# Optimization experiments

Measured on AMD Instinct MI355X. Metric: run time of the kernel, lower is better.

Reference implementation:

```python
import jax, jax.numpy as jnp
import numpy as np

B, S, D, H = 2, 2048, 1024, 16
DK = D // H


def setup_inputs() -> dict:
    key = jax.random.key(0)
    ks = jax.random.split(key, 8)
    Q = jax.random.normal(ks[0], (B, S, D), dtype=jnp.float32)
    K = jax.random.normal(ks[1], (B, S, D), dtype=jnp.float32)
    V = jax.random.normal(ks[2], (B, S, D), dtype=jnp.float32)
    scale = 0.02
    W_q = jax.random.normal(ks[3], (D, D), dtype=jnp.float32) * scale
    W_k = jax.random.normal(ks[4], (D, D), dtype=jnp.float32) * scale
    W_v = jax.random.normal(ks[5], (D, D), dtype=jnp.float32) * scale
    W_o = jax.random.normal(ks[6], (D, D), dtype=jnp.float32) * scale
    b_q = jnp.zeros((D,), jnp.float32)
    b_k = jnp.zeros((D,), jnp.float32)
    b_v = jnp.zeros((D,), jnp.float32)
    b_o = jnp.zeros((D,), jnp.float32)
    # causal mask, broadcastable [1,1,S,S]; mask==0 positions are masked out
    mask = jnp.tril(jnp.ones((S, S), jnp.int32))[None, None, :, :]
    return dict(Q=Q, K=K, V=V, W_q=W_q, b_q=b_q, W_k=W_k, b_k=b_k,
                W_v=W_v, b_v=b_v, W_o=W_o, b_o=b_o, mask=mask)


def reference(Q, K, V, W_q, b_q, W_k, b_k, W_v, b_v, W_o, b_o, mask):
    # linear projections (torch Linear equivalent up to weight layout)
    q = Q @ W_q + b_q   # [B,S,D]
    k = K @ W_k + b_k
    v = V @ W_v + b_v
    # split heads -> [B,H,S,DK]
    q = q.reshape(B, S, H, DK).transpose(0, 2, 1, 3)
    k = k.reshape(B, S, H, DK).transpose(0, 2, 1, 3)
    v = v.reshape(B, S, H, DK).transpose(0, 2, 1, 3)
    # scaled dot-product attention with explicit [B,H,S,S] scores
    scores = jnp.einsum('bhqd,bhkd->bhqk', q, k) / jnp.sqrt(jnp.float32(DK))
    scores = jnp.where(mask == 0, jnp.float32(-1e9), scores)
    attn = jax.nn.softmax(scores, axis=-1)
    out = jnp.einsum('bhqk,bhkd->bhqd', attn, v)
    # merge heads and output projection
    out = out.transpose(0, 2, 1, 3).reshape(B, S, D)
    return out @ W_o + b_o
```

## Files before the change

kernel.cpp:

```cpp
#include <hip/hip_runtime.h>


typedef unsigned short u16;
typedef __attribute__((ext_vector_type(8))) short s8v;
typedef __attribute__((ext_vector_type(4))) float f4v;

#define S_ 2048
#define D_ 1024
#define H_ 16
#define DK_ 64

__device__ __forceinline__ u16 f2bf(float f) {
  unsigned u = __builtin_bit_cast(unsigned, f);
  u += 0x7fffu + ((u >> 16) & 1u);
  return (u16)(u >> 16);
}
__device__ __forceinline__ u16 f2bf_t(float f) {
  return (u16)(__builtin_bit_cast(unsigned, f) >> 16);
}

__device__ __forceinline__ void gld_lds16(const u16* g, u16* l) {
  __builtin_amdgcn_global_load_lds(
      (const __attribute__((address_space(1))) unsigned int*)g,
      (__attribute__((address_space(3))) unsigned int*)l, 16, 0, 0);
}

__global__ __launch_bounds__(256) void prep(
    const float* __restrict__ Q, const float* __restrict__ K, const float* __restrict__ V,
    u16* __restrict__ Qc, u16* __restrict__ Kc, u16* __restrict__ Vc,
    const float* __restrict__ W0, const float* __restrict__ W1,
    const float* __restrict__ W2, const float* __restrict__ W3,
    u16* __restrict__ T0, u16* __restrict__ T1, u16* __restrict__ T2, u16* __restrict__ T3) {
  int bid = blockIdx.x, tid = threadIdx.x;
  if (bid < 3072) {
    int z = bid >> 10, t = bid & 1023;
    const float* s = z == 0 ? Q : z == 1 ? K : V;
    u16*         d = z == 0 ? Qc : z == 1 ? Kc : Vc;
    const int n4 = (2 * S_ * D_) / 4;
    for (int idx = t * 256 + tid; idx < n4; idx += 1024 * 256) {
      float4 f = ((const float4*)s)[idx];
      unsigned lo = (unsigned)f2bf(f.x) | ((unsigned)f2bf(f.y) << 16);
      unsigned hi = (unsigned)f2bf(f.z) | ((unsigned)f2bf(f.w) << 16);
      ((uint2*)d)[idx] = make_uint2(lo, hi);
    }
  } else {
    int wb = bid - 3072;
    int z = wb >> 10, t = wb & 1023;
    const float* W = z == 0 ? W0 : z == 1 ? W1 : z == 2 ? W2 : W3;
    u16*         T = z == 0 ? T0 : z == 1 ? T1 : z == 2 ? T2 : T3;
    __shared__ float tile[32][33];
    int tx = tid & 31, ty = tid >> 5;
    int c0 = (t & 31) * 32, r0 = (t >> 5) * 32;
#pragma unroll
    for (int i = 0; i < 32; i += 8)
      tile[ty + i][tx] = W[(size_t)(r0 + ty + i) * D_ + c0 + tx];
    __syncthreads();
#pragma unroll
    for (int i = 0; i < 32; i += 8)
      T[(size_t)(c0 + ty + i) * D_ + r0 + tx] = f2bf(tile[tx][ty + i]);
  }
}

#define BK_ 64

template <int MI, int NJ, int MODE>
__device__ __forceinline__ void gemm_core(const u16* __restrict__ A, const u16* __restrict__ Bt,
                                          const float* __restrict__ bias, void* __restrict__ out,
                                          float oscale, u16* lds, int m0, int n0) {
  constexpr int BM = MI * 32;
  constexpr int BN = NJ * 32;
  u16* Al = lds;
  u16* Bl = lds + BM * BK_;
  int tid = threadIdx.x;
  int w = tid >> 6, lane = tid & 63, quad = lane >> 4, col = lane & 15;
  int wm = (w >> 1) * (MI * 16), wn = (w & 1) * (NJ * 16);
  f4v acc[MI][NJ] = {};
  const u16* Ag = A + (size_t)m0 * 1024;
  const u16* Bg = Bt + (size_t)n0 * 1024;
  int sr = tid >> 3, ss = tid & 7;

  for (int k0 = 0; k0 < 1024; k0 += BK_) {
    __syncthreads();
#pragma unroll
    for (int c = 0; c < BM / 32; ++c) {
      int r = c * 32 + sr;
      int gs = ss ^ (r & 7);
      gld_lds16(Ag + (size_t)r * 1024 + k0 + gs * 8, &Al[r * BK_ + ss * 8]);
    }
#pragma unroll
    for (int c = 0; c < BN / 32; ++c) {
      int r = c * 32 + sr;
      int gs = ss ^ (r & 7);
      gld_lds16(Bg + (size_t)r * 1024 + k0 + gs * 8, &Bl[r * BK_ + ss * 8]);
    }
    __syncthreads();
#pragma unroll
    for (int hf = 0; hf < 2; ++hf) {
      s8v af[MI], bfr[NJ];
#pragma unroll
      for (int i = 0; i < MI; ++i) {
        int row = wm + i * 16 + col;
        int sl = (hf * 4 + quad) ^ (row & 7);
        af[i] = *(const s8v*)&Al[row * BK_ + sl * 8];
      }
#pragma unroll
      for (int j = 0; j < NJ; ++j) {
        int row = wn + j * 16 + col;
        int sl = (hf * 4 + quad) ^ (row & 7);
        bfr[j] = *(const s8v*)&Bl[row * BK_ + sl * 8];
      }
#pragma unroll
      for (int i = 0; i < MI; ++i)
#pragma unroll
        for (int j = 0; j < NJ; ++j)
          acc[i][j] = __builtin_amdgcn_mfma_f32_16x16x32_bf16(af[i], bfr[j], acc[i][j], 0, 0, 0);
    }
  }

  if (MODE == 1) {
    __syncthreads();
    u16* scr = lds + w * 2304;
    int h = (n0 + wn) >> 6;
    int dkl = lane & 31, sh = (lane >> 5) * 32;
    int mg0 = m0 + wm + sh;
    int bb = mg0 >> 11, s0g = mg0 & 2047;
    u16* ob = (u16*)out + ((size_t)(bb * H_ + h) * DK_) * S_;
#pragma unroll
    for (int t = 0; t < 2; ++t) {
#pragma unroll
      for (int j2 = 2 * t; j2 < 2 * t + 2; ++j2) {
        float bv = bias[n0 + wn + j2 * 16 + col];
        int rloc = j2 * 16 + col - t * 32;
#pragma unroll
        for (int i = 0; i < MI; ++i)
#pragma unroll
          for (int r = 0; r < 4; ++r)
            scr[rloc * 72 + i * 16 + quad * 4 + r] = f2bf(acc[i][j2][r] + bv);
      }
      __builtin_amdgcn_wave_barrier();
      u16* op = ob + (size_t)(t * 32 + dkl) * S_ + s0g;
#pragma unroll
      for (int c = 0; c < 4; ++c)
        *(uint4*)&op[c * 8] = *(const uint4*)&scr[dkl * 72 + sh + c * 8];
      __builtin_amdgcn_wave_barrier();
    }
    return;
  }

#pragma unroll
  for (int i = 0; i < MI; ++i) {
#pragma unroll
    for (int j = 0; j < NJ; ++j) {
      int n = n0 + wn + j * 16 + col;
      float bb = bias[n];
#pragma unroll
      for (int r = 0; r < 4; ++r) {
        int m = m0 + wm + i * 16 + quad * 4 + r;
        float v = (acc[i][j][r] + bb) * oscale;
        if (MODE == 2) {
          ((float*)out)[(size_t)m * 1024 + n] = v;
        } else {
          int b = m >> 11, s = m & 2047, h = n >> 6, dk = n & 63;
          ((u16*)out)[((size_t)(b * H_ + h) * S_ + s) * DK_ + dk] = f2bf(v);
        }
      }
    }
  }
}

#define CEXPQ 0.18033688f

__global__ __launch_bounds__(256, 5) void gemm_qkv(
    const u16* __restrict__ A0, const u16* __restrict__ A1, const u16* __restrict__ A2,
    const u16* __restrict__ B0, const u16* __restrict__ B1, const u16* __restrict__ B2,
    const float* __restrict__ bi0, const float* __restrict__ bi1, const float* __restrict__ bi2,
    u16* __restrict__ o0, u16* __restrict__ o1, u16* __restrict__ o2) {
  __shared__ __attribute__((aligned(16))) u16 lds[128 * BK_ + 128 * BK_];
  int k = blockIdx.x;
  int s = blockIdx.y;
  if (s < 32) {
    int ty = k * 4 + (s >> 3), tx = s & 7;
    gemm_core<4, 4, 1>(A2, B2, bi2, o2, 1.0f, lds, ty * 128, tx * 128);
  } else {
    int q = s - 32;
    int g = q >> 6;
    int r = q & 63;
    int ty = k * 4 + (r >> 4), tx = r & 15;
    if (g == 0)
      gemm_core<4, 2, 0>(A0, B0, bi0, o0, CEXPQ, lds, ty * 128, tx * 64);
    else
      gemm_core<4, 2, 0>(A1, B1, bi1, o1, 1.0f, lds, ty * 128, tx * 64);
  }
}

__global__ __launch_bounds__(256, 6) void gemm_out(const u16* __restrict__ A, const u16* __restrict__ Bt,
                                                   const float* __restrict__ bias, float* __restrict__ out) {
  constexpr int BM = 64, BN = 32;
  constexpr int TILE = (BM + BN) * BK_;
  __shared__ __attribute__((aligned(16))) u16 lds[2 * TILE];
  int k = blockIdx.x;
  int s = blockIdx.y;
  int ty = k * 8 + (s >> 5), tx = s & 31;
  int m0 = ty * 64, n0 = tx * 32;

  int tid = threadIdx.x;
  int w = tid >> 6, lane = tid & 63, quad = lane >> 4, col = lane & 15;
  int wm = (w >> 1) * 32, wn = (w & 1) * 16;
  f4v acc[2][1] = {};
  const u16* Ag = A + (size_t)m0 * 1024;
  const u16* Bg = Bt + (size_t)n0 * 1024;
  int sr = tid >> 3, ss = tid & 7;

  auto stage = [&](int buf, int k0) {
    u16* Al = lds + buf * TILE;
    u16* Bl = Al + BM * BK_;
#pragma unroll
    for (int c = 0; c < BM / 32; ++c) {
      int r = c * 32 + sr;
      int gs = ss ^ (r & 7);
      gld_lds16(Ag + (size_t)r * 1024 + k0 + gs * 8, &Al[r * BK_ + ss * 8]);
    }
    {
      int r = sr;
      int gs = ss ^ (r & 7);
      gld_lds16(Bg + (size_t)r * 1024 + k0 + gs * 8, &Bl[r * BK_ + ss * 8]);
    }
  };

  stage(0, 0);
  int cur = 0;
  for (int k0 = 0; k0 < 1024; k0 += BK_) {
    __syncthreads();
    if (k0 + BK_ < 1024) stage(cur ^ 1, k0 + BK_);
    const u16* Al = lds + cur * TILE;
    const u16* Bl = Al + BM * BK_;
#pragma unroll
    for (int hf = 0; hf < 2; ++hf) {
      s8v af[2], bfr;
#pragma unroll
      for (int i = 0; i < 2; ++i) {
        int row = wm + i * 16 + col;
        int sl = (hf * 4 + quad) ^ (row & 7);
        af[i] = *(const s8v*)&Al[row * BK_ + sl * 8];
      }
      {
        int row = wn + col;
        int sl = (hf * 4 + quad) ^ (row & 7);
        bfr = *(const s8v*)&Bl[row * BK_ + sl * 8];
      }
#pragma unroll
      for (int i = 0; i < 2; ++i)
        acc[i][0] = __builtin_amdgcn_mfma_f32_16x16x32_bf16(af[i], bfr, acc[i][0], 0, 0, 0);
    }
    cur ^= 1;
  }

#pragma unroll
  for (int i = 0; i < 2; ++i) {
    int n = n0 + wn + col;
    float bb = bias[n];
#pragma unroll
    for (int r = 0; r < 4; ++r) {
      int m = m0 + wm + i * 16 + quad * 4 + r;
      out[(size_t)m * 1024 + n] = acc[i][0][r] + bb;
    }
  }
}

#define KT_ 64
#define PSTR 72

__global__ __launch_bounds__(512, 4) void attn_fused(const u16* __restrict__ qb, const u16* __restrict__ kb,
                                                     const u16* __restrict__ vtb, u16* __restrict__ ao) {
  __shared__ __attribute__((aligned(16))) u16 Kt[2][KT_ * PSTR];
  __shared__ __attribute__((aligned(16))) u16 Vts[2][DK_ * PSTR];
  __shared__ __attribute__((aligned(16))) u16 Pl[8][16 * PSTR];
  int xk = blockIdx.x & 7;
  int s = (blockIdx.x >> 3) + 2 * blockIdx.y;
  int pp = s & 31, half = s >> 5;
  int bh_loc = pp & 3, jj = pp >> 2;
  int J = half ? jj : 15 - jj;
  int bh = xk * 4 + bh_loc;
  int b = bh >> 4, h = bh & 15;
  int tid = threadIdx.x, w = tid >> 6, lane = tid & 63, quad = lane >> 4, col = lane & 15;
  int qmin = J * 128 + w * 16;
  int nk = (J + 1) * 128;

  const u16* Qh = qb + (size_t)bh * S_ * DK_;
  const u16* Kh = kb + (size_t)bh * S_ * DK_;
  const u16* Vh = vtb + (size_t)bh * DK_ * S_;

  s8v qf0 = *(const s8v*)(Qh + (size_t)(qmin + col) * DK_ + quad * 8);
  s8v qf1 = *(const s8v*)(Qh + (size_t)(qmin + col) * DK_ + 32 + quad * 8);

  f4v O[4] = {};
  float ls[4] = {};

  int st = tid & 255;
  bool stK = tid < 256;
  int srow = st >> 2, soff = (st & 3) * 16;
  int slo = srow * PSTR + soff;
  const u16* gK = Kh + (size_t)srow * DK_ + soff;
  const u16* gV = Vh + (size_t)srow * S_ + soff;

  uint4 preA, preB;
  {
    const u16* g0 = stK ? gK : gV;
    preA = *(const uint4*)g0;
    preB = *(const uint4*)(g0 + 8);
    u16* d = (stK ? &Kt[0][0] : &Vts[0][0]) + slo;
    *(uint4*)d = preA;
    *(uint4*)(d + 8) = preB;
    const u16* g1 = stK ? gK + (size_t)KT_ * DK_ : gV + KT_;
    preA = *(const uint4*)g1;
    preB = *(const uint4*)(g1 + 8);
  }

  int cur = 0;
  for (int kt = 0; kt < nk; kt += KT_) {
    __syncthreads();
    if (kt + KT_ < nk) {
      u16* d = (stK ? &Kt[cur ^ 1][0] : &Vts[cur ^ 1][0]) + slo;
      *(uint4*)d = preA;
      *(uint4*)(d + 8) = preB;
      int k2 = kt + 2 * KT_;
      if (k2 < nk) {
        const u16* gn = stK ? gK + (size_t)k2 * DK_ : gV + k2;
        preA = *(const uint4*)gn;
        preB = *(const uint4*)(gn + 8);
      }
    }
    if (kt <= qmin + 15) {
      const u16* Kc = &Kt[cur][0];
      const u16* Vc = &Vts[cur][0];

      f4v sc[4];
      __builtin_amdgcn_s_setprio(1);
#pragma unroll
      for (int ks = 0; ks < 4; ++ks) {
        s8v kf0 = *(const s8v*)&Kc[(ks * 16 + col) * PSTR + quad * 8];
        s8v kf1 = *(const s8v*)&Kc[(ks * 16 + col) * PSTR + 32 + quad * 8];
        f4v t = {0.f, 0.f, 0.f, 0.f};
        t = __builtin_amdgcn_mfma_f32_16x16x32_bf16(qf0, kf0, t, 0, 0, 0);
        t = __builtin_amdgcn_mfma_f32_16x16x32_bf16(qf1, kf1, t, 0, 0, 0);
        sc[ks] = t;
      }
      __builtin_amdgcn_s_setprio(0);

      bool full = (kt + KT_ - 1 <= qmin);
#pragma unroll
      for (int r = 0; r < 4; ++r) {
        float p0, p1, p2, p3;
        if (full) {
          p0 = exp2f(sc[0][r]);
          p1 = exp2f(sc[1][r]);
          p2 = exp2f(sc[2][r]);
          p3 = exp2f(sc[3][r]);
        } else {
          int qr = qmin + quad * 4 + r;
          p0 = (kt + col)      <= qr ? exp2f(sc[0][r]) : 0.f;
          p1 = (kt + 16 + col) <= qr ? exp2f(sc[1][r]) : 0.f;
          p2 = (kt + 32 + col) <= qr ? exp2f(sc[2][r]) : 0.f;
          p3 = (kt + 48 + col) <= qr ? exp2f(sc[3][r]) : 0.f;
        }
        ls[r] += (p0 + p1) + (p2 + p3);
        int row = quad * 4 + r;
        Pl[w][row * PSTR + col]      = f2bf_t(p0);
        Pl[w][row * PSTR + 16 + col] = f2bf_t(p1);
        Pl[w][row * PSTR + 32 + col] = f2bf_t(p2);
        Pl[w][row * PSTR + 48 + col] = f2bf_t(p3);
      }
      __builtin_amdgcn_wave_barrier();

      s8v pa0 = *(const s8v*)&Pl[w][col * PSTR + quad * 8];
      s8v pa1 = *(const s8v*)&Pl[w][col * PSTR + 32 + quad * 8];
      __builtin_amdgcn_s_setprio(1);
#pragma unroll
      for (int d = 0; d < 4; ++d) {
        s8v vf0 = *(const s8v*)&Vc[(d * 16 + col) * PSTR + quad * 8];
        s8v vf1 = *(const s8v*)&Vc[(d * 16 + col) * PSTR + 32 + quad * 8];
        O[d] = __builtin_amdgcn_mfma_f32_16x16x32_bf16(pa0, vf0, O[d], 0, 0, 0);
        O[d] = __builtin_amdgcn_mfma_f32_16x16x32_bf16(pa1, vf1, O[d], 0, 0, 0);
      }
      __builtin_amdgcn_s_setprio(0);
      __builtin_amdgcn_wave_barrier();
    }
    cur ^= 1;
  }

#pragma unroll
  for (int r = 0; r < 4; ++r) {
    float l = ls[r];
    l += __shfl_xor(l, 1);
    l += __shfl_xor(l, 2);
    l += __shfl_xor(l, 4);
    l += __shfl_xor(l, 8);
    float inv = 1.0f / l;
    size_t row = (size_t)(b * S_ + qmin + quad * 4 + r);
#pragma unroll
    for (int d = 0; d < 4; ++d)
      ao[row * D_ + h * DK_ + d * 16 + col] = f2bf(O[d][r] * inv);
  }
}

extern "C" void kernel_launch(void* const* d_in, const int* in_sizes, int n_in,
                              void* d_out, int out_size, void* d_ws, size_t ws_size,
                              hipStream_t stream) {
  const float* Q  = (const float*)d_in[0];
  const float* K  = (const float*)d_in[1];
  const float* V  = (const float*)d_in[2];
  const float* Wq = (const float*)d_in[3];
  const float* bq = (const float*)d_in[4];
  const float* Wk = (const float*)d_in[5];
  const float* bk = (const float*)d_in[6];
  const float* Wv = (const float*)d_in[7];
  const float* bv = (const float*)d_in[8];
  const float* Wo = (const float*)d_in[9];
  const float* bo = (const float*)d_in[10];

  char* p = (char*)d_ws;
  const size_t TEN = (size_t)2 * S_ * D_ * 2;
  const size_t WT  = (size_t)D_ * D_ * 2;
  u16* Qc  = (u16*)p; p += TEN;
  u16* Kc  = (u16*)p; p += TEN;
  u16* Vc  = (u16*)p; p += TEN;
  u16* Wqt = (u16*)p; p += WT;
  u16* Wkt = (u16*)p; p += WT;
  u16* Wvt = (u16*)p; p += WT;
  u16* Wot = (u16*)p; p += WT;
  u16* qb  = (u16*)p; p += TEN;
  u16* kbf = (u16*)p; p += TEN;
  u16* vtb = (u16*)p; p += TEN;
  u16* ao  = (u16*)p; p += TEN;

  prep<<<7168, 256, 0, stream>>>(Q, K, V, Qc, Kc, Vc, Wq, Wk, Wv, Wo, Wqt, Wkt, Wvt, Wot);
  gemm_qkv<<<dim3(8, 160), 256, 0, stream>>>(Qc, Kc, Vc, Wqt, Wkt, Wvt, bq, bk, bv, qb, kbf, vtb);
  attn_fused<<<dim3(16, 2 * H_), 512, 0, stream>>>(qb, kbf, vtb, ao);
  gemm_out<<<dim3(8, 256), 256, 0, stream>>>(ao, Wot, bo, (float*)d_out);
}
```

Measured before the change: 227.2 us.

## Software-pipeline attention loop: PV of previous tile overlaps QK of current

```diff
diff --git a/kernel.cpp b/kernel.cpp
--- a/kernel.cpp
+++ b/kernel.cpp
@@ -274,7 +274,7 @@
                                                      const u16* __restrict__ vtb, u16* __restrict__ ao) {
   __shared__ __attribute__((aligned(16))) u16 Kt[2][KT_ * PSTR];
   __shared__ __attribute__((aligned(16))) u16 Vts[2][DK_ * PSTR];
-  __shared__ __attribute__((aligned(16))) u16 Pl[8][16 * PSTR];
+  __shared__ __attribute__((aligned(16))) u16 Pl[8][2][16 * PSTR];
   int xk = blockIdx.x & 7;
   int s = (blockIdx.x >> 3) + 2 * blockIdx.y;
   int pp = s & 31, half = s >> 5;
@@ -285,6 +285,7 @@
   int tid = threadIdx.x, w = tid >> 6, lane = tid & 63, quad = lane >> 4, col = lane & 15;
   int qmin = J * 128 + w * 16;
   int nk = (J + 1) * 128;
+  int NT = nk >> 6;
 
   const u16* Qh = qb + (size_t)bh * S_ * DK_;
   const u16* Kh = kb + (size_t)bh * S_ * DK_;
@@ -302,39 +303,56 @@
   int slo = srow * PSTR + soff;
   const u16* gK = Kh + (size_t)srow * DK_ + soff;
   const u16* gV = Vh + (size_t)srow * S_ + soff;
+  u16* Plb = &Pl[w][0][0];
 
   uint4 preA, preB;
-  {
-    const u16* g0 = stK ? gK : gV;
-    preA = *(const uint4*)g0;
-    preB = *(const uint4*)(g0 + 8);
-    u16* d = (stK ? &Kt[0][0] : &Vts[0][0]) + slo;
+  if (stK) {
+    preA = *(const uint4*)gK;
+    preB = *(const uint4*)(gK + 8);
+    u16* d = &Kt[0][0] + slo;
     *(uint4*)d = preA;
     *(uint4*)(d + 8) = preB;
-    const u16* g1 = stK ? gK + (size_t)KT_ * DK_ : gV + KT_;
+    const u16* g1 = gK + (size_t)KT_ * DK_;
     preA = *(const uint4*)g1;
     preB = *(const uint4*)(g1 + 8);
-  }
-
-  int cur = 0;
-  for (int kt = 0; kt < nk; kt += KT_) {
-    __syncthreads();
-    if (kt + KT_ < nk) {
-      u16* d = (stK ? &Kt[cur ^ 1][0] : &Vts[cur ^ 1][0]) + slo;
+  } else {
+    preA = *(const uint4*)gV;
+    preB = *(const uint4*)(gV + 8);
+  }
+
+  for (int T = 0; T < NT; ++T) {
+    int kt = T << 6;
+    int cur = T & 1;
+    __syncthreads();
+
+    if (stK) {
+      if (T + 1 < NT) {
+        u16* d = &Kt[cur ^ 1][0] + slo;
+        *(uint4*)d = preA;
+        *(uint4*)(d + 8) = preB;
+        if (T + 2 < NT) {
+          const u16* gn = gK + (size_t)(kt + 2 * KT_) * DK_;
+          preA = *(const uint4*)gn;
+          preB = *(const uint4*)(gn + 8);
+        }
+      }
+    } else {
+      u16* d = &Vts[cur ^ 1][0] + slo;
       *(uint4*)d = preA;
       *(uint4*)(d + 8) = preB;
-      int k2 = kt + 2 * KT_;
-      if (k2 < nk) {
-        const u16* gn = stK ? gK + (size_t)k2 * DK_ : gV + k2;
+      if (T + 1 < NT) {
+        const u16* gn = gV + kt + KT_;
         preA = *(const uint4*)gn;
         preB = *(const uint4*)(gn + 8);
       }
     }
-    if (kt <= qmin + 15) {
+
+    bool qkg = (kt <= qmin + 15);
+    bool pvg = (T >= 1) && (kt - KT_ <= qmin + 15);
+
+    f4v sc[4];
+    if (qkg) {
       const u16* Kc = &Kt[cur][0];
-      const u16* Vc = &Vts[cur][0];
-
-      f4v sc[4];
       __builtin_amdgcn_s_setprio(1);
 #pragma unroll
       for (int ks = 0; ks < 4; ++ks) {
@@ -346,7 +364,26 @@
         sc[ks] = t;
       }
       __builtin_amdgcn_s_setprio(0);
-
+    }
+
+    if (pvg) {
+      const u16* Vc = &Vts[cur][0];
+      const u16* Plp = Plb + ((T - 1) & 1) * (16 * PSTR);
+      s8v pa0 = *(const s8v*)&Plp[col * PSTR + quad * 8];
+      s8v pa1 = *(const s8v*)&Plp[col * PSTR + 32 + quad * 8];
+      __builtin_amdgcn_s_setprio(1);
+#pragma unroll
+      for (int d = 0; d < 4; ++d) {
+        s8v vf0 = *(const s8v*)&Vc[(d * 16 + col) * PSTR + quad * 8];
+        s8v vf1 = *(const s8v*)&Vc[(d * 16 + col) * PSTR + 32 + quad * 8];
+        O[d] = __builtin_amdgcn_mfma_f32_16x16x32_bf16(pa0, vf0, O[d], 0, 0, 0);
+        O[d] = __builtin_amdgcn_mfma_f32_16x16x32_bf16(pa1, vf1, O[d], 0, 0, 0);
+      }
+      __builtin_amdgcn_s_setprio(0);
+    }
+
+    if (qkg) {
+      u16* Plc = Plb + (T & 1) * (16 * PSTR);
       bool full = (kt + KT_ - 1 <= qmin);
 #pragma unroll
       for (int r = 0; r < 4; ++r) {
@@ -365,27 +402,27 @@
         }
         ls[r] += (p0 + p1) + (p2 + p3);
         int row = quad * 4 + r;
-        Pl[w][row * PSTR + col]      = f2bf_t(p0);
-        Pl[w][row * PSTR + 16 + col] = f2bf_t(p1);
-        Pl[w][row * PSTR + 32 + col] = f2bf_t(p2);
-        Pl[w][row * PSTR + 48 + col] = f2bf_t(p3);
-      }
-      __builtin_amdgcn_wave_barrier();
-
-      s8v pa0 = *(const s8v*)&Pl[w][col * PSTR + quad * 8];
-      s8v pa1 = *(const s8v*)&Pl[w][col * PSTR + 32 + quad * 8];
-      __builtin_amdgcn_s_setprio(1);
-#pragma unroll
-      for (int d = 0; d < 4; ++d) {
-        s8v vf0 = *(const s8v*)&Vc[(d * 16 + col) * PSTR + quad * 8];
-        s8v vf1 = *(const s8v*)&Vc[(d * 16 + col) * PSTR + 32 + quad * 8];
-        O[d] = __builtin_amdgcn_mfma_f32_16x16x32_bf16(pa0, vf0, O[d], 0, 0, 0);
-        O[d] = __builtin_amdgcn_mfma_f32_16x16x32_bf16(pa1, vf1, O[d], 0, 0, 0);
-      }
-      __builtin_amdgcn_s_setprio(0);
-      __builtin_amdgcn_wave_barrier();
-    }
-    cur ^= 1;
+        Plc[row * PSTR + col]      = f2bf_t(p0);
+        Plc[row * PSTR + 16 + col] = f2bf_t(p1);
+        Plc[row * PSTR + 32 + col] = f2bf_t(p2);
+        Plc[row * PSTR + 48 + col] = f2bf_t(p3);
+      }
+    }
+  }
+
+  __syncthreads();
+  if (nk - KT_ <= qmin + 15) {
+    const u16* Vc = &Vts[NT & 1][0];
+    const u16* Plp = Plb + ((NT - 1) & 1) * (16 * PSTR);
+    s8v pa0 = *(const s8v*)&Plp[col * PSTR + quad * 8];
+    s8v pa1 = *(const s8v*)&Plp[col * PSTR + 32 + quad * 8];
+#pragma unroll
+    for (int d = 0; d < 4; ++d) {
+      s8v vf0 = *(const s8v*)&Vc[(d * 16 + col) * PSTR + quad * 8];
+      s8v vf1 = *(const s8v*)&Vc[(d * 16 + col) * PSTR + 32 + quad * 8];
+      O[d] = __builtin_amdgcn_mfma_f32_16x16x32_bf16(pa0, vf0, O[d], 0, 0, 0);
+      O[d] = __builtin_amdgcn_mfma_f32_16x16x32_bf16(pa1, vf1, O[d], 0, 0, 0);
+    }
   }
 
 #pragma unroll
```

Result: slower. 233.9 us (+2.9%).
